# Kernel optimization log

Hardware: AMD Instinct MI355X
Metric: run time of the kernel (lower is better)

## Reference

```python
import jax, jax.numpy as jnp
import numpy as np

B, T, DIM, HEADS = 4, 2048, 1024, 16
D_K = DIM // HEADS


def setup_inputs() -> dict:
    key = jax.random.key(0)
    ks = jax.random.split(key, 5)
    x = jax.random.normal(ks[0], (B, T, DIM), dtype=jnp.float32)
    # nn.Linear params: weight [out, in], bias [out]
    w_qkv = jax.random.normal(ks[1], (3 * DIM, DIM), dtype=jnp.float32) / np.sqrt(DIM)
    b_qkv = jax.random.normal(ks[2], (3 * DIM,), dtype=jnp.float32) * 0.02
    w_out = jax.random.normal(ks[3], (DIM, DIM), dtype=jnp.float32) / np.sqrt(DIM)
    b_out = jax.random.normal(ks[4], (DIM,), dtype=jnp.float32) * 0.02
    # causal mask, broadcast over batch and heads: [1, 1, T, T]
    mask = jnp.tril(jnp.ones((T, T), dtype=jnp.int32))[None, None]
    return {"x": x, "w_qkv": w_qkv, "b_qkv": b_qkv, "w_out": w_out, "b_out": b_out, "mask": mask}


def reference(x, w_qkv, b_qkv, w_out, b_out, mask):
    Bb, Tt, D = x.shape
    # fused QKV projection: [B,T,3D] -> [3,B,H,T,d_k]
    qkv = (x @ w_qkv.T + b_qkv).reshape(Bb, Tt, 3, HEADS, D_K).transpose(2, 0, 3, 1, 4)
    q, k, v = qkv[0], qkv[1], qkv[2]
    scores = jnp.einsum("bhqd,bhkd->bhqk", q, k) / jnp.sqrt(jnp.float32(D_K))
    scores = jnp.where(mask == 0, -jnp.inf, scores)
    attn = jax.nn.softmax(scores, axis=-1)  # [B,H,T,T]
    context = jnp.einsum("bhqk,bhkd->bhqd", attn, v)
    context = context.transpose(0, 2, 1, 3).reshape(Bb, Tt, D)
    return context @ w_out.T + b_out
```

## Files before the change

kernel.cpp:

```cpp
#include <hip/hip_runtime.h>

typedef unsigned short ushort_t;
typedef __bf16 bf16x8 __attribute__((ext_vector_type(8)));
typedef float f32x4 __attribute__((ext_vector_type(4)));

#define BB 4
#define TT 2048
#define DIMD 1024
#define NH 16
#define DK 64
#define MROWS (BB * TT)
#define NQKV (3 * DIMD)

__device__ __forceinline__ ushort_t f2b(float f) {
  __bf16 h = (__bf16)f;
  union { __bf16 h; ushort_t u; } c; c.h = h; return c.u;
}
__device__ __forceinline__ float fexp2(float x) {
  float r;
  asm("v_exp_f32 %0, %1" : "=v"(r) : "v"(x));
  return r;
}

__device__ __forceinline__ void gload_lds16(const void* g, void* l) {
  __builtin_amdgcn_global_load_lds(
      (const __attribute__((address_space(1))) void*)g,
      (__attribute__((address_space(3))) void*)l,
      16, 0, 0);
}

__global__ __launch_bounds__(256) void cast_f32_bf16(
    const float* __restrict__ in, ushort_t* __restrict__ out, int n)
{
  const int i = (blockIdx.x * 256 + threadIdx.x) * 8;
  if (i >= n) return;
  float4 a = *(const float4*)(in + i);
  float4 b = *(const float4*)(in + i + 4);
  ushort_t o[8];
  o[0] = f2b(a.x); o[1] = f2b(a.y); o[2] = f2b(a.z); o[3] = f2b(a.w);
  o[4] = f2b(b.x); o[5] = f2b(b.y); o[6] = f2b(b.z); o[7] = f2b(b.w);
  *(uint4*)(out + i) = *(const uint4*)o;
}

template <bool OUT_F32>
__global__ __launch_bounds__(512, 4) void gemm_bt_pipe(
    const ushort_t* __restrict__ A, const ushort_t* __restrict__ W,
    const float* __restrict__ bias, void* __restrict__ Cp,
    int M, int N, int K)
{
  __shared__ __align__(16) ushort_t As[3][128 * 32];
  __shared__ __align__(16) ushort_t Bs[3][256 * 32];

  const int tid = threadIdx.x;
  const int wave = tid >> 6, lane = tid & 63;
  const int tiles_n = N >> 8;
  const int nwg = (M >> 7) * tiles_n;
  int bid = blockIdx.x;
  { const int q = nwg >> 3; bid = (bid & 7) * q + (bid >> 3); }
  const int bm = bid / tiles_n, bn = bid % tiles_n;
  const int row0 = bm << 7, col0 = bn << 8;
  const int wm = (wave >> 2) << 6;
  const int wn = (wave & 3) << 6;
  const int fr = lane & 15;
  const int g  = lane >> 4;
  const int g4 = g << 2;
  const int csw = (g ^ (fr >> 2)) << 3;

  const int srow = lane >> 2;
  const int scol = ((lane & 3) ^ ((lane >> 4) & 3)) << 3;
  const int lbase = wave << 9;

  const ushort_t* Ag  = A + (size_t)(row0 + (wave << 4) + srow) * K + scol;
  const ushort_t* Wg0 = W + (size_t)(col0 + (wave << 4) + srow) * K + scol;
  const ushort_t* Wg1 = Wg0 + (size_t)128 * K;

#define STAGE_P(kt, buf)                                                      \
  {                                                                           \
    const size_t _k = (size_t)(kt) << 5;                                      \
    gload_lds16(Ag + _k,  &As[buf][lbase]);                                   \
    gload_lds16(Wg0 + _k, &Bs[buf][lbase]);                                   \
    gload_lds16(Wg1 + _k, &Bs[buf][4096 + lbase]);                            \
  }

  const int NT = K >> 5;
  STAGE_P(0, 0);
  STAGE_P(1, 1);

  f32x4 acc[4][4] = {};
  int cr = 0, st = 2;

  for (int t = 0; t < NT; ++t) {
    if (t + 1 < NT) asm volatile("s_waitcnt vmcnt(3)" ::: "memory");
    else            asm volatile("s_waitcnt vmcnt(0)" ::: "memory");
    __builtin_amdgcn_s_barrier();

    const ushort_t* as_ = As[cr];
    const ushort_t* bs_ = Bs[cr];
    bf16x8 af0 = *(const bf16x8*)&as_[(wm +      fr) * 32 + csw];
    bf16x8 af1 = *(const bf16x8*)&as_[(wm + 16 + fr) * 32 + csw];
    bf16x8 bw0 = *(const bf16x8*)&bs_[(wn +      fr) * 32 + csw];
    bf16x8 bw1 = *(const bf16x8*)&bs_[(wn + 16 + fr) * 32 + csw];
    bf16x8 bw2 = *(const bf16x8*)&bs_[(wn + 32 + fr) * 32 + csw];
    bf16x8 bw3 = *(const bf16x8*)&bs_[(wn + 48 + fr) * 32 + csw];
    if (t + 2 < NT) STAGE_P(t + 2, st);
    asm volatile("s_waitcnt lgkmcnt(0)" ::: "memory");
    __builtin_amdgcn_sched_barrier(0);
    __builtin_amdgcn_s_setprio(1);
    acc[0][0] = __builtin_amdgcn_mfma_f32_16x16x32_bf16(af0, bw0, acc[0][0], 0, 0, 0);
    acc[0][1] = __builtin_amdgcn_mfma_f32_16x16x32_bf16(af0, bw1, acc[0][1], 0, 0, 0);
    acc[0][2] = __builtin_amdgcn_mfma_f32_16x16x32_bf16(af0, bw2, acc[0][2], 0, 0, 0);
    acc[0][3] = __builtin_amdgcn_mfma_f32_16x16x32_bf16(af0, bw3, acc[0][3], 0, 0, 0);
    acc[1][0] = __builtin_amdgcn_mfma_f32_16x16x32_bf16(af1, bw0, acc[1][0], 0, 0, 0);
    acc[1][1] = __builtin_amdgcn_mfma_f32_16x16x32_bf16(af1, bw1, acc[1][1], 0, 0, 0);
    acc[1][2] = __builtin_amdgcn_mfma_f32_16x16x32_bf16(af1, bw2, acc[1][2], 0, 0, 0);
    acc[1][3] = __builtin_amdgcn_mfma_f32_16x16x32_bf16(af1, bw3, acc[1][3], 0, 0, 0);
    __builtin_amdgcn_s_setprio(0);

    bf16x8 af2 = *(const bf16x8*)&as_[(wm + 32 + fr) * 32 + csw];
    bf16x8 af3 = *(const bf16x8*)&as_[(wm + 48 + fr) * 32 + csw];
    asm volatile("s_waitcnt lgkmcnt(0)" ::: "memory");
    __builtin_amdgcn_sched_barrier(0);
    __builtin_amdgcn_s_setprio(1);
    acc[2][0] = __builtin_amdgcn_mfma_f32_16x16x32_bf16(af2, bw0, acc[2][0], 0, 0, 0);
    acc[2][1] = __builtin_amdgcn_mfma_f32_16x16x32_bf16(af2, bw1, acc[2][1], 0, 0, 0);
    acc[2][2] = __builtin_amdgcn_mfma_f32_16x16x32_bf16(af2, bw2, acc[2][2], 0, 0, 0);
    acc[2][3] = __builtin_amdgcn_mfma_f32_16x16x32_bf16(af2, bw3, acc[2][3], 0, 0, 0);
    acc[3][0] = __builtin_amdgcn_mfma_f32_16x16x32_bf16(af3, bw0, acc[3][0], 0, 0, 0);
    acc[3][1] = __builtin_amdgcn_mfma_f32_16x16x32_bf16(af3, bw1, acc[3][1], 0, 0, 0);
    acc[3][2] = __builtin_amdgcn_mfma_f32_16x16x32_bf16(af3, bw2, acc[3][2], 0, 0, 0);
    acc[3][3] = __builtin_amdgcn_mfma_f32_16x16x32_bf16(af3, bw3, acc[3][3], 0, 0, 0);
    __builtin_amdgcn_s_setprio(0);

    ++cr; if (cr == 3) cr = 0;
    ++st; if (st == 3) st = 0;
  }
#undef STAGE_P

#pragma unroll
  for (int j = 0; j < 4; ++j) {
    const int col = col0 + wn + (j << 4) + fr;
    const float bv = bias[col];
#pragma unroll
    for (int i = 0; i < 4; ++i)
#pragma unroll
      for (int r = 0; r < 4; ++r) {
        const size_t row = (size_t)(row0 + wm + (i << 4) + g4 + r);
        if constexpr (OUT_F32)
          ((float*)Cp)[row * (size_t)N + col] = acc[i][j][r] + bv;
        else
          ((ushort_t*)Cp)[row * (size_t)N + col] = f2b(acc[i][j][r] + bv);
      }
  }
}

#define C1 0.18033688011112042f
__global__ __launch_bounds__(512, 4) void attn_fused(
    const ushort_t* __restrict__ qkv, ushort_t* __restrict__ ctx)
{
  __shared__ __align__(16) ushort_t Qs[128 * 64];
  __shared__ __align__(16) ushort_t Ks[2][64 * 64];
  __shared__ __align__(16) ushort_t Vt[64 * 64];
  __shared__ __align__(16) ushort_t Ps[8][16 * 64];

  const int tid = threadIdx.x, wave = tid >> 6, lane = tid & 63;
  const int fr = lane & 15;
  const int g  = lane >> 4;
  const int fk = g << 3;
  const int g4 = g << 2;

  const int bid = blockIdx.x;
  const int bq  = (bid >> 3) & 7;
  const int G   = (bid & 7) | ((bid >> 6) << 3);
  const int h   = G & 15;
  const int b   = G >> 4;

  const int srl = lane >> 3;
  const int scc = ((lane & 7) ^ srl) << 3;
  const int vr  = tid >> 3;
  const int vc  = (tid & 7) << 3;
  const int rsw = (fr & 7) << 3;

  const ushort_t* Kg = qkv + (size_t)b * TT * NQKV + DIMD + h * DK;
  const ushort_t* Vg = qkv + (size_t)b * TT * NQKV + 2 * DIMD + h * DK;

#pragma unroll 1
  for (int t = 0; t < 2; ++t) {
    const int qt = t ? (15 - bq) : bq;
    const int ktmax = 2 * qt + 1;
    const int diag  = 2 * qt + (wave >> 2);
    const size_t qrow0 = (size_t)b * TT + (size_t)qt * 128;

    __syncthreads();

    const ushort_t* Qg = qkv + qrow0 * NQKV + h * DK;
#pragma unroll
    for (int pp = 0; pp < 2; ++pp) {
      const int e  = (wave << 9) + (pp << 12);
      const int rr = (e >> 6) + srl;
      gload_lds16(Qg + (size_t)rr * NQKV + scc, Qs + e);
    }
    {
      const int e  = wave << 9;
      const int rr = (wave << 3) + srl;
      gload_lds16(Kg + (size_t)rr * NQKV + scc, Ks[0] + e);
    }
    uint4 va = *(const uint4*)(Vg + (size_t)vr * NQKV + vc);
    asm volatile("s_waitcnt vmcnt(0)" ::: "memory");
    __syncthreads();

    bf16x8 aqr[2];
#pragma unroll
    for (int ks = 0; ks < 2; ++ks)
      aqr[ks] = *(const bf16x8*)&Qs[((wave << 4) + fr) * 64 + (((ks << 5) + fk) ^ rsw)];

    const int qrow = (qt << 7) + (wave << 4) + fr;
    float mrow = -1e30f, lrow = 0.f;
    f32x4 oacc[4] = {};
    int cur = 0;

    for (int kt = 0; kt <= ktmax; ++kt) {
      {
        __align__(16) ushort_t tmp[8];
        *(uint4*)tmp = va;
#pragma unroll
        for (int j = 0; j < 8; ++j) {
          const int d  = vc + j;
          const int hh = (d & 7) ^ ((d >> 3) & 7);
          Vt[d * 64 + (vr ^ (hh << 3))] = tmp[j];
        }
      }
      if (kt < ktmax) {
        const size_t krow = (size_t)(kt + 1) << 6;
        const int e  = wave << 9;
        const int rr = (wave << 3) + srl;
        gload_lds16(Kg + (krow + rr) * NQKV + scc, Ks[cur ^ 1] + e);
        va = *(const uint4*)(Vg + (krow + vr) * NQKV + vc);
      }
      asm volatile("s_waitcnt lgkmcnt(0)" ::: "memory");
      __builtin_amdgcn_s_barrier();

      if (kt <= diag) {
        f32x4 s[4] = {};
        __builtin_amdgcn_s_setprio(1);
#pragma unroll
        for (int ks = 0; ks < 2; ++ks)
#pragma unroll
          for (int ni = 0; ni < 4; ++ni) {
            const bf16x8 bk = *(const bf16x8*)&Ks[cur][((ni << 4) + fr) * 64 + (((ks << 5) + fk) ^ rsw)];
            s[ni] = __builtin_amdgcn_mfma_f32_16x16x32_bf16(bk, aqr[ks], s[ni], 0, 0, 0);
          }
        __builtin_amdgcn_s_setprio(0);

        if (kt == diag) {
          const int kb = kt << 6;
#pragma unroll
          for (int ni = 0; ni < 4; ++ni)
#pragma unroll
            for (int r = 0; r < 4; ++r) {
              const int kc = kb + (ni << 4) + g4 + r;
              if (kc > qrow) s[ni][r] = -1e30f;
            }
        }

        float rm = -1e30f;
#pragma unroll
        for (int ni = 0; ni < 4; ++ni) {
          const float m01 = fmaxf(s[ni][0], s[ni][1]);
          const float m23 = fmaxf(s[ni][2], s[ni][3]);
          rm = fmaxf(rm, fmaxf(m01, m23));
        }
        rm = fmaxf(rm, __shfl_xor(rm, 16, 64));
        rm = fmaxf(rm, __shfl_xor(rm, 32, 64));

        if (__any(rm > mrow + 64.f)) {
          const float mn = fmaxf(mrow, rm);
          const float corr = fexp2((mrow - mn) * C1);
          mrow = mn;
          lrow *= corr;
#pragma unroll
          for (int ni = 0; ni < 4; ++ni) oacc[ni] *= corr;
        }
        const float nm2 = -mrow * C1;
        float rs = 0.f;
#pragma unroll
        for (int ni = 0; ni < 4; ++ni)
#pragma unroll
          for (int r = 0; r < 4; ++r) {
            const float pe = fexp2(fmaf(s[ni][r], C1, nm2));
            s[ni][r] = pe;
            rs += pe;
          }
        rs += __shfl_xor(rs, 16, 64);
        rs += __shfl_xor(rs, 32, 64);
        lrow += rs;

#pragma unroll
        for (int ni = 0; ni < 4; ++ni) {
          ushort_t o4[4];
#pragma unroll
          for (int r = 0; r < 4; ++r) o4[r] = f2b(s[ni][r]);
          *(uint2*)&Ps[wave][fr * 64 + (((ni << 4) + g4) ^ rsw)] = *(const uint2*)o4;
        }
        asm volatile("s_waitcnt lgkmcnt(0)" ::: "memory");
        __builtin_amdgcn_sched_barrier(0);

        __builtin_amdgcn_s_setprio(1);
#pragma unroll
        for (int ks = 0; ks < 2; ++ks) {
          const bf16x8 ap = *(const bf16x8*)&Ps[wave][fr * 64 + (((ks << 5) + fk) ^ rsw)];
#pragma unroll
          for (int ni = 0; ni < 4; ++ni) {
            const int hh = (fr & 7) ^ ((2 * ni + (fr >> 3)) & 7);
            const bf16x8 bv = *(const bf16x8*)&Vt[((ni << 4) + fr) * 64 + (((ks << 5) + fk) ^ (hh << 3))];
            oacc[ni] = __builtin_amdgcn_mfma_f32_16x16x32_bf16(bv, ap, oacc[ni], 0, 0, 0);
          }
        }
        __builtin_amdgcn_s_setprio(0);
      }

      if (kt < ktmax) {
        asm volatile("s_waitcnt vmcnt(0)" ::: "memory");
        __syncthreads();
      }
      cur ^= 1;
    }

    const float inv = 1.f / lrow;
    ushort_t* crow = ctx + (qrow0 + (wave << 4) + fr) * DIMD + h * DK;
#pragma unroll
    for (int ni = 0; ni < 4; ++ni) {
      ushort_t o4[4];
#pragma unroll
      for (int r = 0; r < 4; ++r) o4[r] = f2b(oacc[ni][r] * inv);
      *(uint2*)&crow[(ni << 4) + g4] = *(const uint2*)o4;
    }
  }
}

extern "C" void kernel_launch(void* const* d_in, const int* in_sizes, int n_in,
                              void* d_out, int out_size, void* d_ws, size_t ws_size,
                              hipStream_t stream) {
  const float* x     = (const float*)d_in[0];
  const float* w_qkv = (const float*)d_in[1];
  const float* b_qkv = (const float*)d_in[2];
  const float* w_out = (const float*)d_in[3];
  const float* b_out = (const float*)d_in[4];

  const size_t need = 36u * 1024 * 1024 * sizeof(ushort_t);
  if (ws_size < need) return;

  ushort_t* qkv = (ushort_t*)d_ws;
  ushort_t* xb  = qkv + (size_t)MROWS * NQKV;
  ushort_t* wqb = xb  + (size_t)MROWS * DIMD;
  ushort_t* wob = wqb + (size_t)NQKV * DIMD;
  ushort_t* ctx = xb;
  float*    out = (float*)d_out;

  cast_f32_bf16<<<dim3(MROWS * DIMD / 2048), dim3(256), 0, stream>>>(x, xb, MROWS * DIMD);
  cast_f32_bf16<<<dim3(NQKV * DIMD / 2048), dim3(256), 0, stream>>>(w_qkv, wqb, NQKV * DIMD);
  cast_f32_bf16<<<dim3(DIMD * DIMD / 2048), dim3(256), 0, stream>>>(w_out, wob, DIMD * DIMD);
  gemm_bt_pipe<false><<<dim3((MROWS / 128) * (NQKV / 256)), dim3(512), 0, stream>>>(
      xb, wqb, b_qkv, (void*)qkv, MROWS, NQKV, DIMD);
  attn_fused<<<dim3(BB * NH * 8), dim3(512), 0, stream>>>(qkv, ctx);
  gemm_bt_pipe<true><<<dim3((MROWS / 128) * (DIMD / 256)), dim3(512), 0, stream>>>(
      ctx, wob, b_out, (void*)out, MROWS, DIMD, DIMD);
}
```

Baseline: 176.8 us.

## Double-buffer V tile and overlap K/V prefetch with QK MFMAs in attention

The attention loop gets a double-buffered transposed V tile in shared memory. The next K tile's global-to-LDS load and the V transpose-store are issued after the QK^T MFMAs instead of before them, and the loop drops from two barriers per iteration to one. This is meant to hide global load latency behind compute and cut synchronisation stalls, at the cost of 8 KB more LDS per block. The GEMM's block-index swizzle is also replaced with a fixed mapping that groups 8 row tiles per XCD slot. That mapping assumes M is 64 row tiles.

```diff
diff --git a/kernel.cpp b/kernel.cpp
--- a/kernel.cpp
+++ b/kernel.cpp
@@ -53,11 +53,9 @@
 
   const int tid = threadIdx.x;
   const int wave = tid >> 6, lane = tid & 63;
-  const int tiles_n = N >> 8;
-  const int nwg = (M >> 7) * tiles_n;
-  int bid = blockIdx.x;
-  { const int q = nwg >> 3; bid = (bid & 7) * q + (bid >> 3); }
-  const int bm = bid / tiles_n, bn = bid % tiles_n;
+  const int x = blockIdx.x & 7, j = blockIdx.x >> 3;
+  const int bm = (x << 3) | (j & 7);
+  const int bn = j >> 3;
   const int row0 = bm << 7, col0 = bn << 8;
   const int wm = (wave >> 2) << 6;
   const int wn = (wave & 3) << 6;
@@ -137,8 +135,8 @@
 #undef STAGE_P
 
 #pragma unroll
-  for (int j = 0; j < 4; ++j) {
-    const int col = col0 + wn + (j << 4) + fr;
+  for (int jj = 0; jj < 4; ++jj) {
+    const int col = col0 + wn + (jj << 4) + fr;
     const float bv = bias[col];
 #pragma unroll
     for (int i = 0; i < 4; ++i)
@@ -146,9 +144,9 @@
       for (int r = 0; r < 4; ++r) {
         const size_t row = (size_t)(row0 + wm + (i << 4) + g4 + r);
         if constexpr (OUT_F32)
-          ((float*)Cp)[row * (size_t)N + col] = acc[i][j][r] + bv;
+          ((float*)Cp)[row * (size_t)N + col] = acc[i][jj][r] + bv;
         else
-          ((ushort_t*)Cp)[row * (size_t)N + col] = f2b(acc[i][j][r] + bv);
+          ((ushort_t*)Cp)[row * (size_t)N + col] = f2b(acc[i][jj][r] + bv);
       }
   }
 }
@@ -159,7 +157,7 @@
 {
   __shared__ __align__(16) ushort_t Qs[128 * 64];
   __shared__ __align__(16) ushort_t Ks[2][64 * 64];
-  __shared__ __align__(16) ushort_t Vt[64 * 64];
+  __shared__ __align__(16) ushort_t Vt[2][64 * 64];
   __shared__ __align__(16) ushort_t Ps[8][16 * 64];
 
   const int tid = threadIdx.x, wave = tid >> 6, lane = tid & 63;
@@ -193,6 +191,7 @@
     __syncthreads();
 
     const ushort_t* Qg = qkv + qrow0 * NQKV + h * DK;
+    uint4 va = *(const uint4*)(Vg + (size_t)vr * NQKV + vc);
 #pragma unroll
     for (int pp = 0; pp < 2; ++pp) {
       const int e  = (wave << 9) + (pp << 12);
@@ -204,7 +203,6 @@
       const int rr = (wave << 3) + srl;
       gload_lds16(Kg + (size_t)rr * NQKV + scc, Ks[0] + e);
     }
-    uint4 va = *(const uint4*)(Vg + (size_t)vr * NQKV + vc);
     asm volatile("s_waitcnt vmcnt(0)" ::: "memory");
     __syncthreads();
 
@@ -212,35 +210,34 @@
 #pragma unroll
     for (int ks = 0; ks < 2; ++ks)
       aqr[ks] = *(const bf16x8*)&Qs[((wave << 4) + fr) * 64 + (((ks << 5) + fk) ^ rsw)];
+
+    {
+      __align__(16) ushort_t tmp[8];
+      *(uint4*)tmp = va;
+#pragma unroll
+      for (int jj = 0; jj < 8; ++jj) {
+        const int d  = vc + jj;
+        const int hh = (d & 7) ^ ((d >> 3) & 7);
+        Vt[0][d * 64 + (vr ^ (hh << 3))] = tmp[jj];
+      }
+    }
+    va = *(const uint4*)(Vg + (size_t)(64 + vr) * NQKV + vc);
+    asm volatile("s_waitcnt lgkmcnt(0)" ::: "memory");
 
     const int qrow = (qt << 7) + (wave << 4) + fr;
     float mrow = -1e30f, lrow = 0.f;
     f32x4 oacc[4] = {};
-    int cur = 0;
 
     for (int kt = 0; kt <= ktmax; ++kt) {
-      {
-        __align__(16) ushort_t tmp[8];
-        *(uint4*)tmp = va;
-#pragma unroll
-        for (int j = 0; j < 8; ++j) {
-          const int d  = vc + j;
-          const int hh = (d & 7) ^ ((d >> 3) & 7);
-          Vt[d * 64 + (vr ^ (hh << 3))] = tmp[j];
-        }
-      }
-      if (kt < ktmax) {
-        const size_t krow = (size_t)(kt + 1) << 6;
-        const int e  = wave << 9;
-        const int rr = (wave << 3) + srl;
-        gload_lds16(Kg + (krow + rr) * NQKV + scc, Ks[cur ^ 1] + e);
-        va = *(const uint4*)(Vg + (krow + vr) * NQKV + vc);
-      }
-      asm volatile("s_waitcnt lgkmcnt(0)" ::: "memory");
+      asm volatile("s_waitcnt vmcnt(0)" ::: "memory");
       __builtin_amdgcn_s_barrier();
 
+      const int cur = kt & 1, nxt = cur ^ 1;
+      f32x4 s[4];
+
       if (kt <= diag) {
-        f32x4 s[4] = {};
+#pragma unroll
+        for (int ni = 0; ni < 4; ++ni) s[ni] = f32x4{0.f, 0.f, 0.f, 0.f};
         __builtin_amdgcn_s_setprio(1);
 #pragma unroll
         for (int ks = 0; ks < 2; ++ks)
@@ -250,7 +247,28 @@
             s[ni] = __builtin_amdgcn_mfma_f32_16x16x32_bf16(bk, aqr[ks], s[ni], 0, 0, 0);
           }
         __builtin_amdgcn_s_setprio(0);
-
+      }
+
+      if (kt < ktmax) {
+        const size_t krow = (size_t)(kt + 1) << 6;
+        const int e  = wave << 9;
+        const int rr = (wave << 3) + srl;
+        gload_lds16(Kg + (krow + rr) * NQKV + scc, Ks[nxt] + e);
+        {
+          __align__(16) ushort_t tmp[8];
+          *(uint4*)tmp = va;
+#pragma unroll
+          for (int jj = 0; jj < 8; ++jj) {
+            const int d  = vc + jj;
+            const int hh = (d & 7) ^ ((d >> 3) & 7);
+            Vt[nxt][d * 64 + (vr ^ (hh << 3))] = tmp[jj];
+          }
+        }
+        if (kt + 1 < ktmax)
+          va = *(const uint4*)(Vg + ((size_t)(kt + 2) * 64 + vr) * NQKV + vc);
+      }
+
+      if (kt <= diag) {
         if (kt == diag) {
           const int kb = kt << 6;
 #pragma unroll
@@ -311,18 +329,14 @@
 #pragma unroll
           for (int ni = 0; ni < 4; ++ni) {
             const int hh = (fr & 7) ^ ((2 * ni + (fr >> 3)) & 7);
-            const bf16x8 bv = *(const bf16x8*)&Vt[((ni << 4) + fr) * 64 + (((ks << 5) + fk) ^ (hh << 3))];
+            const bf16x8 bv = *(const bf16x8*)&Vt[cur][((ni << 4) + fr) * 64 + (((ks << 5) + fk) ^ (hh << 3))];
             oacc[ni] = __builtin_amdgcn_mfma_f32_16x16x32_bf16(bv, ap, oacc[ni], 0, 0, 0);
           }
         }
         __builtin_amdgcn_s_setprio(0);
       }
 
-      if (kt < ktmax) {
-        asm volatile("s_waitcnt vmcnt(0)" ::: "memory");
-        __syncthreads();
-      }
-      cur ^= 1;
+      asm volatile("s_waitcnt lgkmcnt(0)" ::: "memory");
     }
 
     const float inv = 1.f / lrow;
```

Result: slower. 182.5 us (+3.2%).

## Switch GEMM to double-buffered LDS with barrier-guarded prefetch and new tile remap

Applied to the files above, without the earlier changes.

The projection GEMM drops from triple to double LDS buffering. All A/B fragments for a k-step are now read up front, then a second barrier runs before the next stage is prefetched into the same buffer. Cutting LDS use is meant to let more workgroups fit per CU. The cost is an extra barrier per k-step and a shorter prefetch distance. The workgroup-to-tile mapping is also replaced with a bit-sliced scheme that groups 8 row tiles per XCD slot, aiming at better cache locality.

```diff
diff --git a/kernel.cpp b/kernel.cpp
--- a/kernel.cpp
+++ b/kernel.cpp
@@ -48,16 +48,14 @@
     const float* __restrict__ bias, void* __restrict__ Cp,
     int M, int N, int K)
 {
-  __shared__ __align__(16) ushort_t As[3][128 * 32];
-  __shared__ __align__(16) ushort_t Bs[3][256 * 32];
+  __shared__ __align__(16) ushort_t As[2][128 * 32];
+  __shared__ __align__(16) ushort_t Bs[2][256 * 32];
 
   const int tid = threadIdx.x;
   const int wave = tid >> 6, lane = tid & 63;
-  const int tiles_n = N >> 8;
-  const int nwg = (M >> 7) * tiles_n;
-  int bid = blockIdx.x;
-  { const int q = nwg >> 3; bid = (bid & 7) * q + (bid >> 3); }
-  const int bm = bid / tiles_n, bn = bid % tiles_n;
+  const int x = blockIdx.x & 7, j = blockIdx.x >> 3;
+  const int bm = (x << 3) | (j & 7);
+  const int bn = j >> 3;
   const int row0 = bm << 7, col0 = bn << 8;
   const int wm = (wave >> 2) << 6;
   const int wn = (wave & 3) << 6;
@@ -87,23 +85,28 @@
   STAGE_P(1, 1);
 
   f32x4 acc[4][4] = {};
-  int cr = 0, st = 2;
 
   for (int t = 0; t < NT; ++t) {
     if (t + 1 < NT) asm volatile("s_waitcnt vmcnt(3)" ::: "memory");
     else            asm volatile("s_waitcnt vmcnt(0)" ::: "memory");
     __builtin_amdgcn_s_barrier();
 
-    const ushort_t* as_ = As[cr];
-    const ushort_t* bs_ = Bs[cr];
+    const int buf = t & 1;
+    const ushort_t* as_ = As[buf];
+    const ushort_t* bs_ = Bs[buf];
     bf16x8 af0 = *(const bf16x8*)&as_[(wm +      fr) * 32 + csw];
     bf16x8 af1 = *(const bf16x8*)&as_[(wm + 16 + fr) * 32 + csw];
+    bf16x8 af2 = *(const bf16x8*)&as_[(wm + 32 + fr) * 32 + csw];
+    bf16x8 af3 = *(const bf16x8*)&as_[(wm + 48 + fr) * 32 + csw];
     bf16x8 bw0 = *(const bf16x8*)&bs_[(wn +      fr) * 32 + csw];
     bf16x8 bw1 = *(const bf16x8*)&bs_[(wn + 16 + fr) * 32 + csw];
     bf16x8 bw2 = *(const bf16x8*)&bs_[(wn + 32 + fr) * 32 + csw];
     bf16x8 bw3 = *(const bf16x8*)&bs_[(wn + 48 + fr) * 32 + csw];
-    if (t + 2 < NT) STAGE_P(t + 2, st);
     asm volatile("s_waitcnt lgkmcnt(0)" ::: "memory");
+    __builtin_amdgcn_s_barrier();
+
+    if (t + 2 < NT) STAGE_P(t + 2, buf);
+
     __builtin_amdgcn_sched_barrier(0);
     __builtin_amdgcn_s_setprio(1);
     acc[0][0] = __builtin_amdgcn_mfma_f32_16x16x32_bf16(af0, bw0, acc[0][0], 0, 0, 0);
@@ -114,13 +117,6 @@
     acc[1][1] = __builtin_amdgcn_mfma_f32_16x16x32_bf16(af1, bw1, acc[1][1], 0, 0, 0);
     acc[1][2] = __builtin_amdgcn_mfma_f32_16x16x32_bf16(af1, bw2, acc[1][2], 0, 0, 0);
     acc[1][3] = __builtin_amdgcn_mfma_f32_16x16x32_bf16(af1, bw3, acc[1][3], 0, 0, 0);
-    __builtin_amdgcn_s_setprio(0);
-
-    bf16x8 af2 = *(const bf16x8*)&as_[(wm + 32 + fr) * 32 + csw];
-    bf16x8 af3 = *(const bf16x8*)&as_[(wm + 48 + fr) * 32 + csw];
-    asm volatile("s_waitcnt lgkmcnt(0)" ::: "memory");
-    __builtin_amdgcn_sched_barrier(0);
-    __builtin_amdgcn_s_setprio(1);
     acc[2][0] = __builtin_amdgcn_mfma_f32_16x16x32_bf16(af2, bw0, acc[2][0], 0, 0, 0);
     acc[2][1] = __builtin_amdgcn_mfma_f32_16x16x32_bf16(af2, bw1, acc[2][1], 0, 0, 0);
     acc[2][2] = __builtin_amdgcn_mfma_f32_16x16x32_bf16(af2, bw2, acc[2][2], 0, 0, 0);
@@ -130,15 +126,12 @@
     acc[3][2] = __builtin_amdgcn_mfma_f32_16x16x32_bf16(af3, bw2, acc[3][2], 0, 0, 0);
     acc[3][3] = __builtin_amdgcn_mfma_f32_16x16x32_bf16(af3, bw3, acc[3][3], 0, 0, 0);
     __builtin_amdgcn_s_setprio(0);
-
-    ++cr; if (cr == 3) cr = 0;
-    ++st; if (st == 3) st = 0;
   }
 #undef STAGE_P
 
 #pragma unroll
-  for (int j = 0; j < 4; ++j) {
-    const int col = col0 + wn + (j << 4) + fr;
+  for (int jj = 0; jj < 4; ++jj) {
+    const int col = col0 + wn + (jj << 4) + fr;
     const float bv = bias[col];
 #pragma unroll
     for (int i = 0; i < 4; ++i)
@@ -146,9 +139,9 @@
       for (int r = 0; r < 4; ++r) {
         const size_t row = (size_t)(row0 + wm + (i << 4) + g4 + r);
         if constexpr (OUT_F32)
-          ((float*)Cp)[row * (size_t)N + col] = acc[i][j][r] + bv;
+          ((float*)Cp)[row * (size_t)N + col] = acc[i][jj][r] + bv;
         else
-          ((ushort_t*)Cp)[row * (size_t)N + col] = f2b(acc[i][j][r] + bv);
+          ((ushort_t*)Cp)[row * (size_t)N + col] = f2b(acc[i][jj][r] + bv);
       }
   }
 }
@@ -223,10 +216,10 @@
         __align__(16) ushort_t tmp[8];
         *(uint4*)tmp = va;
 #pragma unroll
-        for (int j = 0; j < 8; ++j) {
-          const int d  = vc + j;
+        for (int jj = 0; jj < 8; ++jj) {
+          const int d  = vc + jj;
           const int hh = (d & 7) ^ ((d >> 3) & 7);
-          Vt[d * 64 + (vr ^ (hh << 3))] = tmp[j];
+          Vt[d * 64 + (vr ^ (hh << 3))] = tmp[jj];
         }
       }
       if (kt < ktmax) {
```

Measured after the change: 175.3 us. No clear change (-0.8%).
